# Performance work log

Hardware: AMD Instinct MI355X
Metric: run time of the kernel (lower is better)

The kernel has to match this reference:

```python
import jax, jax.numpy as jnp
import numpy as np

HEADS = 16
LN_EPS = 1e-5


def setup_inputs() -> dict:
    key = jax.random.key(0)
    ks = jax.random.split(key, 8)
    B, S, D = 2, 2048, 1024
    F = 4 * D
    std = 0.02
    return {
        "x": jax.random.normal(ks[0], (B, S, D), jnp.float32),
        # QKV projections (stored as (in, out)); kaiming-normal-like scale
        "Wq": jax.random.normal(ks[1], (D, D), jnp.float32) * std,
        "bq": jnp.zeros((D,), jnp.float32),
        "Wk": jax.random.normal(ks[2], (D, D), jnp.float32) * std,
        "bk": jnp.zeros((D,), jnp.float32),
        "Wv": jax.random.normal(ks[3], (D, D), jnp.float32) * std,
        "bv": jnp.zeros((D,), jnp.float32),
        # FFN
        "W1": jax.random.normal(ks[4], (D, F), jnp.float32) * std,
        "b1": jnp.zeros((F,), jnp.float32),
        "W2": jax.random.normal(ks[5], (F, D), jnp.float32) * std,
        "b2": jnp.zeros((D,), jnp.float32),
        # LayerNorm
        "gamma": jnp.ones((D,), jnp.float32),
        "beta": jnp.zeros((D,), jnp.float32),
    }


def reference(x, Wq, bq, Wk, bk, Wv, bv, W1, b1, W2, b2, gamma, beta):
    B, S, D = x.shape
    H = HEADS
    hd = D // H
    # QKV projections -> [B, H, S, hd]
    Q = (x @ Wq + bq).reshape(B, S, H, hd).transpose(0, 2, 1, 3)
    K = (x @ Wk + bk).reshape(B, S, H, hd).transpose(0, 2, 1, 3)
    V = (x @ Wv + bv).reshape(B, S, H, hd).transpose(0, 2, 1, 3)
    # scores scaled by sqrt(embedding_dim), faithful to source (not head_dim)
    scores = jnp.einsum('bhqd,bhkd->bhqk', Q, K) / jnp.sqrt(jnp.asarray(D, x.dtype))
    attn = jax.nn.softmax(scores, axis=-1)
    # diagonal_training: zero the diagonal of the post-softmax attention matrix
    attn = attn * (1.0 - jnp.eye(S, dtype=attn.dtype))
    out = jnp.einsum('bhqk,bhkd->bhqd', attn, V)
    out = out.transpose(0, 2, 1, 3).reshape(B, S, D)
    # dropout is identity in eval mode
    h = jax.nn.gelu(out @ W1 + b1, approximate=False) @ W2 + b2
    # LayerNorm
    mu = jnp.mean(h, axis=-1, keepdims=True)
    var = jnp.var(h, axis=-1, keepdims=True)
    return (h - mu) * jax.lax.rsqrt(var + LN_EPS) * gamma + beta
```

## Files before the change

### kernel.cpp

```cpp
#include <hip/hip_runtime.h>

using bf16x8 = __attribute__((ext_vector_type(8))) short;
using f32x4  = __attribute__((ext_vector_type(4))) float;

__device__ __forceinline__ float b2f(ushort u) {
  union { unsigned int i; float f; } v; v.i = ((unsigned int)u) << 16; return v.f;
}
__device__ __forceinline__ ushort f2b(float f) {
  unsigned int x = __float_as_uint(f);
  unsigned int r = (x + 0x7FFFu + ((x >> 16) & 1u)) >> 16;
  return (ushort)r;
}
__device__ __forceinline__ unsigned cvt_pk_bf16(float a, float b) {
  unsigned r;
  asm("v_cvt_pk_bf16_f32 %0, %1, %2" : "=v"(r) : "v"(a), "v"(b));
  return r;
}

__device__ __forceinline__ void gld_lds16(const void* g, void* l) {
  __builtin_amdgcn_global_load_lds(
      (const __attribute__((address_space(1))) void*)g,
      (__attribute__((address_space(3))) void*)l, 16, 0, 0);
}


__global__ void cast_bf16_kernel(const float* __restrict__ in, ushort* __restrict__ out, int n) {
  int i = (blockIdx.x * blockDim.x + threadIdx.x) * 4;
  if (i < n) {
    float4 v = *(const float4*)(in + i);
    ushort4 o = make_ushort4(f2b(v.x), f2b(v.y), f2b(v.z), f2b(v.w));
    *(ushort4*)(out + i) = o;
  }
}

__global__ void transpose_cast_kernel(const float* __restrict__ in, ushort* __restrict__ out,
                                      int R, int C) {
  __shared__ float tile[32][33];
  int tx = threadIdx.x, ty = threadIdx.y;
  int cb = blockIdx.x * 32, rb = blockIdx.y * 32;
  for (int i = ty; i < 32; i += 8)
    tile[i][tx] = in[(size_t)(rb + i) * C + (cb + tx)];
  __syncthreads();
  for (int i = ty; i < 32; i += 8)
    out[(size_t)(cb + i) * R + (rb + tx)] = f2b(tile[tx][i]);
}

__global__ void transpose_v_kernel(const ushort* __restrict__ V, ushort* __restrict__ Vt) {
  __shared__ ushort t[32][33];
  int bh = blockIdx.z;
  int b = bh >> 4, h = bh & 15;
  int s0 = blockIdx.x * 32, d0 = blockIdx.y * 32;
  const ushort* Vbp = V + ((size_t)b * 2048) * 1024 + h * 64;
  ushort* Vtb = Vt + (size_t)bh * 64 * 2048;
  int tx = threadIdx.x, ty = threadIdx.y;
  for (int i = ty; i < 32; i += 8) t[i][tx] = Vbp[(size_t)(s0 + i) * 1024 + d0 + tx];
  __syncthreads();
  for (int i = ty; i < 32; i += 8) Vtb[(size_t)(d0 + i) * 2048 + s0 + tx] = t[tx][i];
}


template<int EPI>
__global__ __launch_bounds__(512) void gemm256(
    const ushort* __restrict__ A, const ushort* __restrict__ Bt,
    const float* __restrict__ bias, void* __restrict__ Cout,
    int M, int N, int K)
{
  extern __shared__ ushort lds[];

  const int nwg = gridDim.x * gridDim.y;
  const int bid = blockIdx.y * gridDim.x + blockIdx.x;
  const int cpx = nwg >> 3;
  const int swz = (bid & 7) * cpx + (bid >> 3);
  const int bm = (swz % gridDim.x) * 256;
  const int bn = (swz / gridDim.x) * 256;

  const int tid = threadIdx.x;
  const int lane = tid & 63, w = tid >> 6;
  const int wr = w >> 2, wc = w & 3;
  const int hi = lane >> 4, c = lane & 15;

  const int srow = tid >> 2;
  const int scol = (tid & 3) * 8;
  const int soff = srow * 32 + scol;
  const ushort* gA0 = A  + (size_t)(bm + srow) * K + scol;
  const ushort* gA1 = gA0 + (size_t)128 * K;
  const ushort* gB0 = Bt + (size_t)(bn + srow) * K + scol;
  const ushort* gB1 = gB0 + (size_t)128 * K;

  const int NT = K / 32;
  f32x4 acc[8][4] = {};

  auto STAGE = [&](int buf, int t) {
    ushort* bA = lds + buf * 16384;
    ushort* bB = bA + 8192;
    const size_t ko = (size_t)t * 32;
    gld_lds16(gA0 + ko, bA + soff);
    gld_lds16(gA1 + ko, bA + 4096 + soff);
    gld_lds16(gB0 + ko, bB + soff);
    gld_lds16(gB1 + ko, bB + 4096 + soff);
  };

  STAGE(0, 0);
  __syncthreads();

  int cur = 0;
  for (int t = 0; t < NT; ++t) {
    if (t + 1 < NT) STAGE(cur ^ 1, t + 1);
    const ushort* sA = lds + cur * 16384;
    const ushort* sB = sA + 8192;
    bf16x8 bf[4], af[8];
    #pragma unroll
    for (int n = 0; n < 4; ++n)
      bf[n] = *(const bf16x8*)&sB[(wc * 64 + n * 16 + c) * 32 + hi * 8];
    #pragma unroll
    for (int m = 0; m < 8; ++m)
      af[m] = *(const bf16x8*)&sA[(wr * 128 + m * 16 + c) * 32 + hi * 8];
    __builtin_amdgcn_s_setprio(1);
    #pragma unroll
    for (int m = 0; m < 8; ++m)
      #pragma unroll
      for (int n = 0; n < 4; ++n)
        acc[m][n] = __builtin_amdgcn_mfma_f32_16x16x32_bf16(af[m], bf[n], acc[m][n], 0, 0, 0);
    __builtin_amdgcn_s_setprio(0);
    __syncthreads();
    cur ^= 1;
  }

  ushort* eb = &lds[w * 1088];
  const int g = hi;
  const int er = lane >> 3;
  const int es = (lane & 7) * 8;
  float bia[4];
  #pragma unroll
  for (int n = 0; n < 4; ++n) bia[n] = bias[bn + wc * 64 + n * 16 + c];

  #pragma unroll
  for (int mf = 0; mf < 8; ++mf) {
    #pragma unroll
    for (int n = 0; n < 4; ++n) {
      #pragma unroll
      for (int r = 0; r < 4; ++r) {
        float v = acc[mf][n][r] + bia[n];
        if (EPI == 1) {
          float u = 0.7978845608028654f * (v + 0.044715f * v * v * v);
          float au = fabsf(u);
          float e = __expf(-2.0f * au);
          float th = (1.0f - e) / (1.0f + e);
          th = copysignf(th, u);
          v = 0.5f * v * (1.0f + th);
        }
        eb[(g * 4 + r) * 68 + n * 16 + c] = f2b(v);
      }
    }
    asm volatile("" ::: "memory");
    bf16x8 v0 = *(const bf16x8*)&eb[er * 68 + es];
    bf16x8 v1 = *(const bf16x8*)&eb[(er + 8) * 68 + es];
    int grow = bm + wr * 128 + mf * 16 + er;
    int gcol = bn + wc * 64 + es;
    if (EPI == 3) {
      ushort* dst = (ushort*)Cout + (size_t)(gcol >> 10) * 4194304 + (gcol & 1023);
      *(bf16x8*)(dst + (size_t)grow * 1024) = v0;
      *(bf16x8*)(dst + (size_t)(grow + 8) * 1024) = v1;
    } else {
      ushort* dst = (ushort*)Cout + gcol;
      *(bf16x8*)(dst + (size_t)grow * N) = v0;
      *(bf16x8*)(dst + (size_t)(grow + 8) * N) = v1;
    }
    asm volatile("" ::: "memory");
  }
}


#define BM 128
#define BN 128
#define BK 32

__global__ __launch_bounds__(256) void gemm_bf16_f32(
    const ushort* __restrict__ A, const ushort* __restrict__ Bt,
    float* __restrict__ C0, float* __restrict__ C1,
    float* __restrict__ C2, float* __restrict__ C3,
    int M, int N, int Kstride, int k_len)
{
  __shared__ ushort Asm_[2][BM * BK];
  __shared__ ushort Bsm_[2][BN * BK];
  const int bm = blockIdx.x * BM, bn = blockIdx.y * BN;
  const int k_begin = blockIdx.z * k_len;
  const int tid = threadIdx.x;
  const int lane = tid & 63, w = tid >> 6;
  const int wm = (w >> 1) * 64, wn = (w & 1) * 64;
  const int g = lane >> 4, c = lane & 15;
  const int swz8 = ((g ^ ((c >> 1) & 3)) * 8);
  const int srow = tid >> 2;
  const int scol = (((tid & 3) ^ ((srow >> 1) & 3)) * 8);
  const int soff = srow * 32 + (tid & 3) * 8;

  const ushort* gA0 = A  + (size_t)(bm + srow) * Kstride + k_begin + scol;
  const ushort* gA1 = gA0 + (size_t)64 * Kstride;
  const ushort* gB0 = Bt + (size_t)(bn + srow) * Kstride + k_begin + scol;
  const ushort* gB1 = gB0 + (size_t)64 * Kstride;

  f32x4 acc[4][4] = {};
  const int nt = k_len / BK;

  gld_lds16(gA0, &Asm_[0][soff]);
  gld_lds16(gA1, &Asm_[0][64 * 32 + soff]);
  gld_lds16(gB0, &Bsm_[0][soff]);
  gld_lds16(gB1, &Bsm_[0][64 * 32 + soff]);
  __syncthreads();

  int cur = 0;
  for (int t = 0; t < nt; ++t) {
    if (t + 1 < nt) {
      int k0 = (t + 1) * BK;
      gld_lds16(gA0 + k0, &Asm_[cur ^ 1][soff]);
      gld_lds16(gA1 + k0, &Asm_[cur ^ 1][64 * 32 + soff]);
      gld_lds16(gB0 + k0, &Bsm_[cur ^ 1][soff]);
      gld_lds16(gB1 + k0, &Bsm_[cur ^ 1][64 * 32 + soff]);
    }
    bf16x8 af[4], bfr[4];
    #pragma unroll
    for (int m = 0; m < 4; ++m)
      af[m] = *(const bf16x8*)&Asm_[cur][(wm + m * 16 + c) * 32 + swz8];
    #pragma unroll
    for (int n = 0; n < 4; ++n)
      bfr[n] = *(const bf16x8*)&Bsm_[cur][(wn + n * 16 + c) * 32 + swz8];
    #pragma unroll
    for (int m = 0; m < 4; ++m)
      #pragma unroll
      for (int n = 0; n < 4; ++n)
        acc[m][n] = __builtin_amdgcn_mfma_f32_16x16x32_bf16(af[m], bfr[n], acc[m][n], 0, 0, 0);
    __syncthreads();
    cur ^= 1;
  }

  float* dst = C0;
  if (blockIdx.z == 1) dst = C1;
  else if (blockIdx.z == 2) dst = C2;
  else if (blockIdx.z == 3) dst = C3;

  #pragma unroll
  for (int n = 0; n < 4; ++n) {
    int col = bn + wn + n * 16 + c;
    #pragma unroll
    for (int m = 0; m < 4; ++m)
      #pragma unroll
      for (int r = 0; r < 4; ++r) {
        int row = bm + wm + m * 16 + g * 4 + r;
        dst[(size_t)row * N + col] = acc[m][n][r];
      }
  }
}


#define ATT_SC2 0.0450842202f

__global__ __launch_bounds__(512) void attn_kernel(
    const ushort* __restrict__ Q, const ushort* __restrict__ K,
    const ushort* __restrict__ V, const ushort* __restrict__ Vt,
    ushort* __restrict__ Out)
{
  const int bid = blockIdx.x;
  const int tile = (bid & 7) * 64 + (bid >> 3);
  const int bh = tile >> 4;
  const int q0 = (tile & 15) * 128;
  const int b = bh >> 4, h = bh & 15;
  const int tid = threadIdx.x;
  const int w = tid >> 6, lane = tid & 63;
  const int hi = lane >> 4, c = lane & 15;
  const int qw = q0 + w * 16;

  const size_t boff = ((size_t)b * 2048) * 1024 + h * 64;
  const ushort* Qp = Q + boff;
  const ushort* Kp = K + boff;
  const ushort* Vp = V + boff;
  const ushort* Vtb = Vt + (size_t)bh * 64 * 2048;

  __shared__ ushort Ksm[2][64 * 64];
  __shared__ ushort Vsm[2][64 * 64];
  __shared__ ushort Psm[8][16 * 72];

  const int srow = tid >> 3;
  const int sslot = tid & 7;
  const int scolx = ((sslot ^ (srow & 7)) * 8);
  const ushort* gK = Kp + (size_t)srow * 1024 + scolx;
  const ushort* gV = Vtb + (size_t)srow * 2048 + scolx;

  bf16x8 qf0 = *(const bf16x8*)(Qp + (size_t)(qw + c) * 1024 + hi * 8);
  bf16x8 qf1 = *(const bf16x8*)(Qp + (size_t)(qw + c) * 1024 + 32 + hi * 8);
  {
    ushort* q0p = (ushort*)&qf0;
    ushort* q1p = (ushort*)&qf1;
    #pragma unroll
    for (int j = 0; j < 8; ++j) {
      q0p[j] = f2b(b2f(q0p[j]) * ATT_SC2);
      q1p[j] = f2b(b2f(q1p[j]) * ATT_SC2);
    }
  }

  f32x4 acc[4] = {};
  float m_run = -1e30f, l_run = 0.f;

  gld_lds16(gK, &Ksm[0][tid * 8]);
  gld_lds16(gV, &Vsm[0][tid * 8]);
  __syncthreads();

  const int nt = 2048 / 64;
  for (int t = 0; t < nt; ++t) {
    const int buf = t & 1;
    if (t + 1 < nt) {
      gld_lds16(gK + (size_t)(t + 1) * 64 * 1024, &Ksm[buf ^ 1][tid * 8]);
      gld_lds16(gV + (size_t)(t + 1) * 64,        &Vsm[buf ^ 1][tid * 8]);
    }

    f32x4 sv[4];
    __builtin_amdgcn_s_setprio(1);
    #pragma unroll
    for (int sub = 0; sub < 4; ++sub) {
      int rr = sub * 16 + c;
      int sw = (rr & 7) * 8;
      bf16x8 k0 = *(const bf16x8*)&Ksm[buf][rr * 64 + ((hi * 8) ^ sw)];
      bf16x8 k1 = *(const bf16x8*)&Ksm[buf][rr * 64 + ((32 + hi * 8) ^ sw)];
      f32x4 z = {};
      z = __builtin_amdgcn_mfma_f32_16x16x32_bf16(k0, qf0, z, 0, 0, 0);
      z = __builtin_amdgcn_mfma_f32_16x16x32_bf16(k1, qf1, z, 0, 0, 0);
      sv[sub] = z;
    }
    __builtin_amdgcn_s_setprio(0);

    float tm = -1e30f;
    #pragma unroll
    for (int sub = 0; sub < 4; ++sub)
      #pragma unroll
      for (int r = 0; r < 4; ++r) tm = fmaxf(tm, sv[sub][r]);
    tm = fmaxf(tm, __shfl_xor(tm, 16));
    tm = fmaxf(tm, __shfl_xor(tm, 32));

    if (!__all(tm <= m_run + 8.0f)) {
      float mnew = fmaxf(m_run, tm);
      float f = exp2f(m_run - mnew);
      l_run *= f;
      #pragma unroll
      for (int r = 0; r < 4; ++r) {
        float fr = __shfl(f, hi * 4 + r, 16);
        #pragma unroll
        for (int dsub = 0; dsub < 4; ++dsub) acc[dsub][r] *= fr;
      }
      m_run = mnew;
    }

    float p[16];
    float psum = 0.f;
    #pragma unroll
    for (int sub = 0; sub < 4; ++sub)
      #pragma unroll
      for (int r = 0; r < 4; ++r) { float e = exp2f(sv[sub][r] - m_run); p[sub * 4 + r] = e; psum += e; }
    psum += __shfl_xor(psum, 16);
    psum += __shfl_xor(psum, 32);
    l_run += psum;

    #pragma unroll
    for (int sub = 0; sub < 4; ++sub) {
      uint2 pk;
      pk.x = cvt_pk_bf16(p[sub * 4 + 0], p[sub * 4 + 1]);
      pk.y = cvt_pk_bf16(p[sub * 4 + 2], p[sub * 4 + 3]);
      *(uint2*)&Psm[w][c * 72 + sub * 16 + hi * 4] = pk;
    }
    asm volatile("" ::: "memory");

    bf16x8 pa0 = *(const bf16x8*)&Psm[w][c * 72 + hi * 8];
    bf16x8 pa1 = *(const bf16x8*)&Psm[w][c * 72 + 32 + hi * 8];
    __builtin_amdgcn_s_setprio(1);
    #pragma unroll
    for (int dsub = 0; dsub < 4; ++dsub) {
      int rr = dsub * 16 + c;
      int sw = (rr & 7) * 8;
      bf16x8 v0 = *(const bf16x8*)&Vsm[buf][rr * 64 + ((hi * 8) ^ sw)];
      bf16x8 v1 = *(const bf16x8*)&Vsm[buf][rr * 64 + ((32 + hi * 8) ^ sw)];
      acc[dsub] = __builtin_amdgcn_mfma_f32_16x16x32_bf16(pa0, v0, acc[dsub], 0, 0, 0);
      acc[dsub] = __builtin_amdgcn_mfma_f32_16x16x32_bf16(pa1, v1, acc[dsub], 0, 0, 0);
    }
    __builtin_amdgcn_s_setprio(0);

    __syncthreads();
  }

  #pragma unroll
  for (int r = 0; r < 4; ++r) {
    int q = qw + hi * 4 + r;
    float part = 0.f;
    #pragma unroll
    for (int t = 0; t < 4; ++t)
      part += b2f(Qp[(size_t)q * 1024 + c * 4 + t]) * b2f(Kp[(size_t)q * 1024 + c * 4 + t]);
    #pragma unroll
    for (int off = 1; off < 16; off <<= 1) part += __shfl_xor(part, off);
    float mq = __shfl(m_run, hi * 4 + r, 16);
    float lq = __shfl(l_run, hi * 4 + r, 16);
    float pqq = exp2f(part * ATT_SC2 - mq);
    float inv = 1.f / lq;
    #pragma unroll
    for (int dsub = 0; dsub < 4; ++dsub) {
      float vq = b2f(Vp[(size_t)q * 1024 + dsub * 16 + c]);
      float o = (acc[dsub][r] - pqq * vq) * inv;
      Out[((size_t)(b * 2048 + q) * 16 + h) * 64 + dsub * 16 + c] = f2b(o);
    }
  }
}


__global__ __launch_bounds__(256) void ln_kernel(float* __restrict__ h,
                                                 const float* __restrict__ p1,
                                                 const float* __restrict__ p2,
                                                 const float* __restrict__ p3,
                                                 const float* __restrict__ b2,
                                                 const float* __restrict__ gamma,
                                                 const float* __restrict__ beta, int np) {
  int row = blockIdx.x, tid = threadIdx.x;
  float* hr = h + (size_t)row * 1024;
  float4 v = ((const float4*)hr)[tid];
  float4 p = ((const float4*)(p1 + (size_t)row * 1024))[tid];
  float4 bb = ((const float4*)b2)[tid];
  v.x += p.x + bb.x; v.y += p.y + bb.y; v.z += p.z + bb.z; v.w += p.w + bb.w;
  if (np == 4) {
    float4 a = ((const float4*)(p2 + (size_t)row * 1024))[tid];
    float4 d = ((const float4*)(p3 + (size_t)row * 1024))[tid];
    v.x += a.x + d.x; v.y += a.y + d.y; v.z += a.z + d.z; v.w += a.w + d.w;
  }
  float s = v.x + v.y + v.z + v.w;
  #pragma unroll
  for (int off = 1; off < 64; off <<= 1) s += __shfl_xor(s, off);
  __shared__ float red[2][4];
  int wv = tid >> 6, lane = tid & 63;
  if (lane == 0) red[0][wv] = s;
  __syncthreads();
  float mu = (red[0][0] + red[0][1] + red[0][2] + red[0][3]) * (1.0f / 1024.0f);
  float dx = v.x - mu, dy = v.y - mu, dz = v.z - mu, dw = v.w - mu;
  float q = dx * dx + dy * dy + dz * dz + dw * dw;
  #pragma unroll
  for (int off = 1; off < 64; off <<= 1) q += __shfl_xor(q, off);
  if (lane == 0) red[1][wv] = q;
  __syncthreads();
  float var = (red[1][0] + red[1][1] + red[1][2] + red[1][3]) * (1.0f / 1024.0f);
  float is = rsqrtf(var + 1e-5f);
  float4 gm = ((const float4*)gamma)[tid];
  float4 bt = ((const float4*)beta)[tid];
  float4 o;
  o.x = dx * is * gm.x + bt.x;
  o.y = dy * is * gm.y + bt.y;
  o.z = dz * is * gm.z + bt.z;
  o.w = dw * is * gm.w + bt.w;
  ((float4*)hr)[tid] = o;
}


extern "C" void kernel_launch(void* const* d_in, const int* in_sizes, int n_in,
                              void* d_out, int out_size, void* d_ws, size_t ws_size,
                              hipStream_t stream) {
  const float* x  = (const float*)d_in[0];
  const float* Wq = (const float*)d_in[1];
  const float* bq = (const float*)d_in[2];
  const float* Wk = (const float*)d_in[3];
  const float* bk = (const float*)d_in[4];
  const float* Wv = (const float*)d_in[5];
  const float* bv = (const float*)d_in[6];
  const float* W1 = (const float*)d_in[7];
  const float* b1 = (const float*)d_in[8];
  const float* W2 = (const float*)d_in[9];
  const float* b2 = (const float*)d_in[10];
  const float* gamma = (const float*)d_in[11];
  const float* beta  = (const float*)d_in[12];
  float* out = (float*)d_out;

  char* ws = (char*)d_ws;
  const size_t MB = 1u << 20;
  ushort* xb    = (ushort*)(ws + 0);
  ushort* Wqkvt = (ushort*)(ws + 8 * MB);
  ushort* Qb    = (ushort*)(ws + 14 * MB);
  ushort* Kb    = (ushort*)(ws + 22 * MB);
  ushort* Vb    = (ushort*)(ws + 30 * MB);
  ushort* Vt    = (ushort*)(ws + 38 * MB);
  ushort* AO    = (ushort*)(ws + 46 * MB);
  ushort* W1t   = (ushort*)(ws + 54 * MB);
  ushort* h1    = (ushort*)(ws + 0);
  ushort* W2t   = (ushort*)(ws + 32 * MB);
  float*  p1    = (float*)(ws + 40 * MB);
  float*  p2    = (float*)(ws + 56 * MB);
  float*  p3    = (float*)(ws + 72 * MB);
  float*  bqkv  = (float*)(ws + 46 * MB);

  const bool split4 = (ws_size >= (size_t)89 * MB);

  (void)hipMemcpyAsync(bqkv,        bq, 4096, hipMemcpyDeviceToDevice, stream);
  (void)hipMemcpyAsync(bqkv + 1024, bk, 4096, hipMemcpyDeviceToDevice, stream);
  (void)hipMemcpyAsync(bqkv + 2048, bv, 4096, hipMemcpyDeviceToDevice, stream);

  dim3 tb(32, 8);
  cast_bf16_kernel<<<4096, 256, 0, stream>>>(x, xb, 4194304);
  transpose_cast_kernel<<<dim3(32, 32), tb, 0, stream>>>(Wq, Wqkvt, 1024, 1024);
  transpose_cast_kernel<<<dim3(32, 32), tb, 0, stream>>>(Wk, Wqkvt + 1024 * 1024, 1024, 1024);
  transpose_cast_kernel<<<dim3(32, 32), tb, 0, stream>>>(Wv, Wqkvt + 2 * 1024 * 1024, 1024, 1024);
  transpose_cast_kernel<<<dim3(128, 32), tb, 0, stream>>>(W1, W1t, 1024, 4096);

  gemm256<3><<<dim3(16, 12), 512, 65536, stream>>>(xb, Wqkvt, bqkv, Qb, 4096, 3072, 1024);

  transpose_v_kernel<<<dim3(64, 2, 32), tb, 0, stream>>>(Vb, Vt);

  attn_kernel<<<512, 512, 0, stream>>>(Qb, Kb, Vb, Vt, AO);

  transpose_cast_kernel<<<dim3(32, 128), tb, 0, stream>>>(W2, W2t, 4096, 1024);

  gemm256<1><<<dim3(16, 16), 512, 65536, stream>>>(AO, W1t, b1, h1, 4096, 4096, 1024);

  if (split4) {
    gemm_bf16_f32<<<dim3(32, 8, 4), 256, 0, stream>>>(h1, W2t, out, p1, p2, p3,
                                                      4096, 1024, 4096, 1024);
    ln_kernel<<<4096, 256, 0, stream>>>(out, p1, p2, p3, b2, gamma, beta, 4);
  } else {
    gemm_bf16_f32<<<dim3(32, 8, 2), 256, 0, stream>>>(h1, W2t, out, p1, nullptr, nullptr,
                                                      4096, 1024, 4096, 2048);
    ln_kernel<<<4096, 256, 0, stream>>>(out, p1, nullptr, nullptr, b2, gamma, beta, 2);
  }
}
```

Before: 257.5 us.

## Shrink QKV and FFN1 GEMM tiles to 128x128 with XOR-swizzled LDS

Replaces the 256x256 tile, 512-thread GEMM with a 128x128 tile, 256-thread version using static LDS. The source column of each global-to-LDS load is XOR-swizzled and the fragment reads use the matching swizzle, to cut LDS bank conflicts. Smaller tiles give four times as many workgroups, which should fill the CUs better and allow more than one block per CU. The cost is lower arithmetic intensity per tile and more global/L2 traffic.

After: 263.9 us. +2.5%, slower.

```diff
diff --git a/kernel.cpp b/kernel.cpp
--- a/kernel.cpp
+++ b/kernel.cpp
@@ -60,82 +60,80 @@
 
 
 template<int EPI>
-__global__ __launch_bounds__(512) void gemm256(
+__global__ __launch_bounds__(256) void gemm128(
     const ushort* __restrict__ A, const ushort* __restrict__ Bt,
     const float* __restrict__ bias, void* __restrict__ Cout,
     int M, int N, int K)
 {
-  extern __shared__ ushort lds[];
+  __shared__ ushort Asm_[2][128 * 32];
+  __shared__ ushort Bsm_[2][128 * 32];
 
   const int nwg = gridDim.x * gridDim.y;
   const int bid = blockIdx.y * gridDim.x + blockIdx.x;
   const int cpx = nwg >> 3;
   const int swz = (bid & 7) * cpx + (bid >> 3);
-  const int bm = (swz % gridDim.x) * 256;
-  const int bn = (swz / gridDim.x) * 256;
+  const int bm = (swz % gridDim.x) * 128;
+  const int bn = (swz / gridDim.x) * 128;
 
   const int tid = threadIdx.x;
   const int lane = tid & 63, w = tid >> 6;
-  const int wr = w >> 2, wc = w & 3;
-  const int hi = lane >> 4, c = lane & 15;
-
+  const int wm = (w >> 1) * 64, wn = (w & 1) * 64;
+  const int g = lane >> 4, c = lane & 15;
+  const int swz8 = ((g ^ ((c >> 1) & 3)) * 8);
   const int srow = tid >> 2;
-  const int scol = (tid & 3) * 8;
-  const int soff = srow * 32 + scol;
+  const int scol = (((tid & 3) ^ ((srow >> 1) & 3)) * 8);
+  const int soff = srow * 32 + (tid & 3) * 8;
+
   const ushort* gA0 = A  + (size_t)(bm + srow) * K + scol;
-  const ushort* gA1 = gA0 + (size_t)128 * K;
+  const ushort* gA1 = gA0 + (size_t)64 * K;
   const ushort* gB0 = Bt + (size_t)(bn + srow) * K + scol;
-  const ushort* gB1 = gB0 + (size_t)128 * K;
-
-  const int NT = K / 32;
-  f32x4 acc[8][4] = {};
-
-  auto STAGE = [&](int buf, int t) {
-    ushort* bA = lds + buf * 16384;
-    ushort* bB = bA + 8192;
-    const size_t ko = (size_t)t * 32;
-    gld_lds16(gA0 + ko, bA + soff);
-    gld_lds16(gA1 + ko, bA + 4096 + soff);
-    gld_lds16(gB0 + ko, bB + soff);
-    gld_lds16(gB1 + ko, bB + 4096 + soff);
-  };
-
-  STAGE(0, 0);
+  const ushort* gB1 = gB0 + (size_t)64 * K;
+
+  f32x4 acc[4][4] = {};
+  const int nt = K / 32;
+
+  gld_lds16(gA0, &Asm_[0][soff]);
+  gld_lds16(gA1, &Asm_[0][64 * 32 + soff]);
+  gld_lds16(gB0, &Bsm_[0][soff]);
+  gld_lds16(gB1, &Bsm_[0][64 * 32 + soff]);
   __syncthreads();
 
   int cur = 0;
-  for (int t = 0; t < NT; ++t) {
-    if (t + 1 < NT) STAGE(cur ^ 1, t + 1);
-    const ushort* sA = lds + cur * 16384;
-    const ushort* sB = sA + 8192;
-    bf16x8 bf[4], af[8];
+  for (int t = 0; t < nt; ++t) {
+    if (t + 1 < nt) {
+      int k0 = (t + 1) * 32;
+      gld_lds16(gA0 + k0, &Asm_[cur ^ 1][soff]);
+      gld_lds16(gA1 + k0, &Asm_[cur ^ 1][64 * 32 + soff]);
+      gld_lds16(gB0 + k0, &Bsm_[cur ^ 1][soff]);
+      gld_lds16(gB1 + k0, &Bsm_[cur ^ 1][64 * 32 + soff]);
+    }
+    bf16x8 af[4], bfr[4];
+    #pragma unroll
+    for (int m = 0; m < 4; ++m)
+      af[m] = *(const bf16x8*)&Asm_[cur][(wm + m * 16 + c) * 32 + swz8];
     #pragma unroll
     for (int n = 0; n < 4; ++n)
-      bf[n] = *(const bf16x8*)&sB[(wc * 64 + n * 16 + c) * 32 + hi * 8];
-    #pragma unroll
-    for (int m = 0; m < 8; ++m)
-      af[m] = *(const bf16x8*)&sA[(wr * 128 + m * 16 + c) * 32 + hi * 8];
+      bfr[n] = *(const bf16x8*)&Bsm_[cur][(wn + n * 16 + c) * 32 + swz8];
     __builtin_amdgcn_s_setprio(1);
     #pragma unroll
-    for (int m = 0; m < 8; ++m)
+    for (int m = 0; m < 4; ++m)
       #pragma unroll
       for (int n = 0; n < 4; ++n)
-        acc[m][n] = __builtin_amdgcn_mfma_f32_16x16x32_bf16(af[m], bf[n], acc[m][n], 0, 0, 0);
+        acc[m][n] = __builtin_amdgcn_mfma_f32_16x16x32_bf16(af[m], bfr[n], acc[m][n], 0, 0, 0);
     __builtin_amdgcn_s_setprio(0);
     __syncthreads();
     cur ^= 1;
   }
 
-  ushort* eb = &lds[w * 1088];
-  const int g = hi;
+  ushort* eb = (ushort*)Asm_ + w * 1088;
   const int er = lane >> 3;
   const int es = (lane & 7) * 8;
   float bia[4];
   #pragma unroll
-  for (int n = 0; n < 4; ++n) bia[n] = bias[bn + wc * 64 + n * 16 + c];
+  for (int n = 0; n < 4; ++n) bia[n] = bias[bn + wn + n * 16 + c];
 
   #pragma unroll
-  for (int mf = 0; mf < 8; ++mf) {
+  for (int mf = 0; mf < 4; ++mf) {
     #pragma unroll
     for (int n = 0; n < 4; ++n) {
       #pragma unroll
@@ -155,8 +153,8 @@
     asm volatile("" ::: "memory");
     bf16x8 v0 = *(const bf16x8*)&eb[er * 68 + es];
     bf16x8 v1 = *(const bf16x8*)&eb[(er + 8) * 68 + es];
-    int grow = bm + wr * 128 + mf * 16 + er;
-    int gcol = bn + wc * 64 + es;
+    int grow = bm + wm + mf * 16 + er;
+    int gcol = bn + wn + es;
     if (EPI == 3) {
       ushort* dst = (ushort*)Cout + (size_t)(gcol >> 10) * 4194304 + (gcol & 1023);
       *(bf16x8*)(dst + (size_t)grow * 1024) = v0;
@@ -500,7 +498,7 @@
   transpose_cast_kernel<<<dim3(32, 32), tb, 0, stream>>>(Wv, Wqkvt + 2 * 1024 * 1024, 1024, 1024);
   transpose_cast_kernel<<<dim3(128, 32), tb, 0, stream>>>(W1, W1t, 1024, 4096);
 
-  gemm256<3><<<dim3(16, 12), 512, 65536, stream>>>(xb, Wqkvt, bqkv, Qb, 4096, 3072, 1024);
+  gemm128<3><<<dim3(32, 24), 256, 0, stream>>>(xb, Wqkvt, bqkv, Qb, 4096, 3072, 1024);
 
   transpose_v_kernel<<<dim3(64, 2, 32), tb, 0, stream>>>(Vb, Vt);
 
@@ -508,7 +506,7 @@
 
   transpose_cast_kernel<<<dim3(32, 128), tb, 0, stream>>>(W2, W2t, 4096, 1024);
 
-  gemm256<1><<<dim3(16, 16), 512, 65536, stream>>>(AO, W1t, b1, h1, 4096, 4096, 1024);
+  gemm128<1><<<dim3(32, 32), 256, 0, stream>>>(AO, W1t, b1, h1, 4096, 4096, 1024);
 
   if (split4) {
     gemm_bf16_f32<<<dim3(32, 8, 4), 256, 0, stream>>>(h1, W2t, out, p1, p2, p3,
```
